# Kernel optimization log

Hardware: AMD Instinct MI355X
Metric: run time of the kernel (lower is better)

The kernel has to match this reference:

```python
import jax, jax.numpy as jnp
import numpy as np

B, T, H, HOR = 512, 256, 256, 22  # batch, seq_len, hidden_size, horizon
IN = 1


def _linear_params(key, fan_in, fan_out):
    kw, kb = jax.random.split(key)
    s = 1.0 / np.sqrt(fan_in)
    w = jax.random.uniform(kw, (fan_in, fan_out), minval=-s, maxval=s, dtype=jnp.float32)
    b = jax.random.uniform(kb, (fan_out,), minval=-s, maxval=s, dtype=jnp.float32)
    return w, b


def setup_inputs() -> dict:
    key = jax.random.key(0)
    ks = jax.random.split(key, 12)
    x = jax.random.normal(ks[0], (B, T, IN), dtype=jnp.float32)
    Wz_w, Wz_b = _linear_params(ks[1], IN, H)
    Uz_w, Uz_b = _linear_params(ks[2], H, H)
    Wr_w, Wr_b = _linear_params(ks[3], IN, H)
    Ur_w, Ur_b = _linear_params(ks[4], H, H)
    Wh_w, Wh_b = _linear_params(ks[5], IN, H)
    Uh_w, Uh_b = _linear_params(ks[6], H, H)
    Wg_w, Wg_b = _linear_params(ks[7], 1, H)
    fc1_w, fc1_b = _linear_params(ks[8], H, H)
    fc2_w, _ = _linear_params(ks[9], H, HOR)
    fc2_w = fc2_w * 0.1                      # model init scales output weight by 0.1
    fc2_b = jnp.full((HOR,), -5.0, dtype=jnp.float32)  # bias.fill_(-5.0)
    return {
        "x": x,
        "Wz_w": Wz_w, "Wz_b": Wz_b, "Uz_w": Uz_w, "Uz_b": Uz_b,
        "Wr_w": Wr_w, "Wr_b": Wr_b, "Ur_w": Ur_w, "Ur_b": Ur_b,
        "Wh_w": Wh_w, "Wh_b": Wh_b, "Uh_w": Uh_w, "Uh_b": Uh_b,
        "Wg_w": Wg_w, "Wg_b": Wg_b,
        "omega_raw": jnp.float32(-8.0), "alpha_raw": jnp.float32(1.0),
        "beta_raw": jnp.float32(1.0), "gamma": jnp.float32(0.4),
        "fc1_w": fc1_w, "fc1_b": fc1_b, "fc2_w": fc2_w, "fc2_b": fc2_b,
    }


def reference(x, Wz_w, Wz_b, Uz_w, Uz_b, Wr_w, Wr_b, Ur_w, Ur_b,
              Wh_w, Wh_b, Uh_w, Uh_b, Wg_w, Wg_b,
              omega_raw, alpha_raw, beta_raw, gamma,
              fc1_w, fc1_b, fc2_w, fc2_b):
    batch = x.shape[0]
    # GARCH reparameterization: omega>0, alpha>=0, beta>=0, alpha+beta<1
    omega = jax.nn.softplus(omega_raw) + 1e-6
    a = jax.nn.sigmoid(alpha_raw)
    b = jax.nn.sigmoid(beta_raw) * (1.0 - a * 0.99)

    # Precompute all input-to-hidden projections (no recurrence dependence)
    xz = jnp.einsum('bti,ih->bth', x, Wz_w) + Wz_b  # (B,T,H)
    xr = jnp.einsum('bti,ih->bth', x, Wr_w) + Wr_b
    xh = jnp.einsum('bti,ih->bth', x, Wh_w) + Wh_b
    eps_seq = x[:, :, 0]                            # (B,T)

    def step(carry, inp):
        h, eps_sq, sig_sq = carry
        xz_t, xr_t, xh_t, eps_t = inp
        garch_in = omega + a * eps_sq + b * sig_sq           # (B,)
        gt = garch_in[:, None] * Wg_w[0] + Wg_b              # Wg: Linear(1,H)
        z = jax.nn.sigmoid(xz_t + h @ Uz_w + Uz_b)
        r = jax.nn.sigmoid(xr_t + h @ Ur_w + Ur_b)
        h_tilde = jnp.tanh(xh_t + (r * h) @ Uh_w + Uh_b)
        h_hat = (1.0 - z) * h_tilde + z * h
        h_new = jnp.tanh(h_hat + gamma * gt)
        return (h_new, eps_t ** 2, garch_in), None

    h0 = jnp.zeros((batch, H), dtype=x.dtype)
    eps0 = jnp.full((batch,), 1e-6, dtype=x.dtype)
    sig0 = jnp.full((batch,), 1e-6, dtype=x.dtype)
    inputs = (jnp.swapaxes(xz, 0, 1), jnp.swapaxes(xr, 0, 1),
              jnp.swapaxes(xh, 0, 1), jnp.swapaxes(eps_seq, 0, 1))
    (h, _, sigma_sq), _ = jax.lax.scan(step, (h0, eps0, sig0), inputs)

    vol_base = jnp.sqrt(sigma_sq + 1e-8)                 # (B,)
    hid = jax.nn.relu(h @ fc1_w + fc1_b)                 # dropout = identity (eval)
    nn_scale = jax.nn.softplus(hid @ fc2_w + fc2_b)      # (B,HOR)
    vol = vol_base[:, None] * (1.0 + nn_scale)
    vol = jnp.clip(vol, 0.01, 10.0)
    return vol, sigma_sq
```

## Files before the change

kernel.cpp:

```cpp
#include <hip/hip_runtime.h>

#define BATCH 512
#define TT 256
#define HH 256
#define HOR 22

__device__ __forceinline__ float bf16lo(unsigned u) { return __uint_as_float(u << 16); }
__device__ __forceinline__ float bf16hi(unsigned u) { return __uint_as_float(u & 0xFFFF0000u); }
__device__ __forceinline__ float rcp_(float x) { return __builtin_amdgcn_rcpf(x); }
__device__ __forceinline__ float sigmoidf_(float x) { return rcp_(1.0f + __expf(-x)); }
__device__ __forceinline__ float tanhf_(float x) {
    float e = __expf(-2.0f * fabsf(x));
    float t = (1.0f - e) * rcp_(1.0f + e);
    return copysignf(t, x);
}
__device__ __forceinline__ unsigned f2bf_rne(float f) {
    unsigned u = __float_as_uint(f);
    unsigned lsb = (u >> 16) & 1u;
    return (u + 0x7FFFu + lsb) >> 16;
}

#define DOT2(acc, a, b) asm("v_dot2_f32_bf16 %0, %1, %2, %0" : "+v"(acc) : "v"(a), "v"(b))

#define PIN(v) asm volatile("" : "+v"(v))
#define PIN4(q) { PIN((q).x); PIN((q).y); PIN((q).z); PIN((q).w); }

#define DPPF(x, ctrl) __int_as_float(__builtin_amdgcn_update_dpp(0, __float_as_int(x), (ctrl), 0xF, 0xF, true))
#define RCOMB(out, a, b, p, ctrl)                          \
    {                                                      \
        float _ta = (a) + DPPF((a), ctrl);                 \
        float _tb = (b) + DPPF((b), ctrl);                 \
        (out) = (p) ? _tb : _ta;                           \
    }
#define RCOMB4(out, a, b, p2v)                                         \
    {                                                                  \
        float _xa = (p2v) ? DPPF((a), 0x114) : DPPF((a), 0x104);       \
        float _xb = (p2v) ? DPPF((b), 0x114) : DPPF((b), 0x104);       \
        float _ta = (a) + _xa;                                         \
        float _tb = (b) + _xb;                                         \
        (out) = (p2v) ? _tb : _ta;                                     \
    }

__global__ __launch_bounds__(256) void prep_kernel(const float* __restrict__ Uz,
                                                   const float* __restrict__ Ur,
                                                   const float* __restrict__ Uh,
                                                   unsigned* __restrict__ UzT,
                                                   unsigned* __restrict__ UrT,
                                                   unsigned* __restrict__ UhT) {
    int tid = blockIdx.x * 256 + threadIdx.x;
    int m  = tid >> 15;
    int r  = tid & 32767;
    int j  = r & 255;
    int kp = r >> 8;
    const float* src = (m == 0) ? Uz : (m == 1) ? Ur : Uh;
    unsigned*    dst = (m == 0) ? UzT : (m == 1) ? UrT : UhT;
    float a0 = src[(2 * kp)     * HH + j];
    float a1 = src[(2 * kp + 1) * HH + j];
    dst[j * (HH / 2) + kp] = f2bf_rne(a0) | (f2bf_rne(a1) << 16);
}

__global__ __launch_bounds__(512) __attribute__((amdgpu_waves_per_eu(2, 2))) void gru_kernel(
    const float* __restrict__ x,
    const float* __restrict__ Wzw, const float* __restrict__ Wzb, const float* __restrict__ Uzb,
    const float* __restrict__ Wrw, const float* __restrict__ Wrb, const float* __restrict__ Urb,
    const float* __restrict__ Whw, const float* __restrict__ Whb, const float* __restrict__ Uhb,
    const float* __restrict__ Wgw, const float* __restrict__ Wgb,
    const float* __restrict__ om_raw, const float* __restrict__ al_raw,
    const float* __restrict__ be_raw, const float* __restrict__ gam,
    const float* __restrict__ fc1w, const float* __restrict__ fc1b,
    const float* __restrict__ fc2w, const float* __restrict__ fc2b,
    const unsigned* __restrict__ UzT, const unsigned* __restrict__ UrT,
    const unsigned* __restrict__ UhT,
    float* __restrict__ out) {
    __shared__ __align__(16) unsigned char hS[2 * 640];
    __shared__ __align__(16) unsigned char rhS[2 * 640];
    __shared__ float xs[2][TT];
    __shared__ float hid[2][HH];

    const int t  = threadIdx.x;
    const int s  = t & 7;
    const int cq = t >> 3;
    const bool p0 = (t & 1), p1 = (t & 2), p2 = (t & 4);
    const int c_own   = t & 3;
    const int b_own   = (t >> 2) & 1;
    const int col_own = 4 * cq + c_own;
    const int b0 = blockIdx.x * 2;

    uint4 wz[4][4], wr[4][4], wh[4][4];
#pragma unroll
    for (int l = 0; l < 4; ++l) {
        const int base = (4 * cq + l) * 128 + s * 16;
        const uint4* pz = (const uint4*)(UzT + base);
        const uint4* pr = (const uint4*)(UrT + base);
        const uint4* ph = (const uint4*)(UhT + base);
#pragma unroll
        for (int u = 0; u < 4; ++u) { wz[l][u] = pz[u]; wr[l][u] = pr[u]; wh[l][u] = ph[u]; }
    }
#pragma unroll
    for (int l = 0; l < 4; ++l) {
#pragma unroll
        for (int u = 0; u < 4; ++u) { PIN4(wz[l][u]); PIN4(wr[l][u]); PIN4(wh[l][u]); }
    }

    const float omega = log1pf(__expf(om_raw[0])) + 1e-6f;
    const float aco   = sigmoidf_(al_raw[0]);
    const float bco   = sigmoidf_(be_raw[0]) * (1.0f - aco * 0.99f);
    const float gma   = gam[0];

    const float wz_o = Wzw[col_own], bz_o = Wzb[col_own] + Uzb[col_own];
    const float wr_o = Wrw[col_own], br_o = Wrb[col_own] + Urb[col_own];
    const float wh_o = Whw[col_own], bh_o = Whb[col_own] + Uhb[col_own];
    const float wg_o = Wgw[col_own], bg_o = Wgb[col_own];

    xs[t >> 8][t & 255] = x[(b0 + (t >> 8)) * TT + (t & 255)];
    if (t < 320) ((unsigned*)hS)[t] = 0;

    float h_own = 0.f, z_own = 0.f;
    float eps0 = 1e-6f, sig0 = 1e-6f, eps1 = 1e-6f, sig1 = 1e-6f;
    __syncthreads();

    const int sl_off = s * 80;
    const int wr_off = (col_own >> 5) * 40 + (col_own & 31);

    for (int tt = 0; tt < TT; ++tt) {
        const float x0 = xs[0][tt];
        const float x1 = xs[1][tt];
        const float g0 = omega + aco * eps0 + bco * sig0;
        const float g1 = omega + aco * eps1 + bco * sig1;
        eps0 = x0 * x0; sig0 = g0;
        eps1 = x1 * x1; sig1 = g1;
        const float x_o = p2 ? x1 : x0;
        const float g_o = p2 ? g1 : g0;

        uint4 ha[4], hb[4];
        {
            const uint4* h0p = (const uint4*)(hS + sl_off);
            const uint4* h1p = (const uint4*)(hS + 640 + sl_off);
#pragma unroll
            for (int u = 0; u < 4; ++u) { ha[u] = h0p[u]; hb[u] = h1p[u]; }
        }
        float az[4][2], ar[4][2];
#pragma unroll
        for (int l = 0; l < 4; ++l) { az[l][0] = 0.f; az[l][1] = 0.f; ar[l][0] = 0.f; ar[l][1] = 0.f; }
#pragma unroll
        for (int l = 0; l < 4; ++l) {
#pragma unroll
            for (int u = 0; u < 4; ++u) {
                uint4 a = wz[l][u], b = wr[l][u];
                DOT2(az[l][0], a.x, ha[u].x); DOT2(az[l][0], a.y, ha[u].y);
                DOT2(az[l][0], a.z, ha[u].z); DOT2(az[l][0], a.w, ha[u].w);
                DOT2(az[l][1], a.x, hb[u].x); DOT2(az[l][1], a.y, hb[u].y);
                DOT2(az[l][1], a.z, hb[u].z); DOT2(az[l][1], a.w, hb[u].w);
                DOT2(ar[l][0], b.x, ha[u].x); DOT2(ar[l][0], b.y, ha[u].y);
                DOT2(ar[l][0], b.z, ha[u].z); DOT2(ar[l][0], b.w, ha[u].w);
                DOT2(ar[l][1], b.x, hb[u].x); DOT2(ar[l][1], b.y, hb[u].y);
                DOT2(ar[l][1], b.z, hb[u].z); DOT2(ar[l][1], b.w, hb[u].w);
            }
        }
        float z1a[2][2], r1a[2][2];
        RCOMB(z1a[0][0], az[0][0], az[1][0], p0, 0xB1);
        RCOMB(z1a[0][1], az[0][1], az[1][1], p0, 0xB1);
        RCOMB(z1a[1][0], az[2][0], az[3][0], p0, 0xB1);
        RCOMB(z1a[1][1], az[2][1], az[3][1], p0, 0xB1);
        RCOMB(r1a[0][0], ar[0][0], ar[1][0], p0, 0xB1);
        RCOMB(r1a[0][1], ar[0][1], ar[1][1], p0, 0xB1);
        RCOMB(r1a[1][0], ar[2][0], ar[3][0], p0, 0xB1);
        RCOMB(r1a[1][1], ar[2][1], ar[3][1], p0, 0xB1);
        float z2a[2], r2a[2];
        RCOMB(z2a[0], z1a[0][0], z1a[1][0], p1, 0x4E);
        RCOMB(z2a[1], z1a[0][1], z1a[1][1], p1, 0x4E);
        RCOMB(r2a[0], r1a[0][0], r1a[1][0], p1, 0x4E);
        RCOMB(r2a[1], r1a[0][1], r1a[1][1], p1, 0x4E);
        float accZ, accR;
        RCOMB4(accZ, z2a[0], z2a[1], p2);
        RCOMB4(accR, r2a[0], r2a[1], p2);

        z_own = sigmoidf_(accZ + x_o * wz_o + bz_o);
        const float r = sigmoidf_(accR + x_o * wr_o + br_o);
        ((unsigned short*)(rhS + b_own * 640))[wr_off] = (unsigned short)f2bf_rne(r * h_own);
        __syncthreads();

        uint4 pa[4], pb[4];
        {
            const uint4* r0p = (const uint4*)(rhS + sl_off);
            const uint4* r1p = (const uint4*)(rhS + 640 + sl_off);
#pragma unroll
            for (int u = 0; u < 4; ++u) { pa[u] = r0p[u]; pb[u] = r1p[u]; }
        }
        float ah[4][2];
#pragma unroll
        for (int l = 0; l < 4; ++l) { ah[l][0] = 0.f; ah[l][1] = 0.f; }
#pragma unroll
        for (int l = 0; l < 4; ++l) {
#pragma unroll
            for (int u = 0; u < 4; ++u) {
                uint4 a = wh[l][u];
                DOT2(ah[l][0], a.x, pa[u].x); DOT2(ah[l][0], a.y, pa[u].y);
                DOT2(ah[l][0], a.z, pa[u].z); DOT2(ah[l][0], a.w, pa[u].w);
                DOT2(ah[l][1], a.x, pb[u].x); DOT2(ah[l][1], a.y, pb[u].y);
                DOT2(ah[l][1], a.z, pb[u].z); DOT2(ah[l][1], a.w, pb[u].w);
            }
        }
        float h1a[2][2];
        RCOMB(h1a[0][0], ah[0][0], ah[1][0], p0, 0xB1);
        RCOMB(h1a[0][1], ah[0][1], ah[1][1], p0, 0xB1);
        RCOMB(h1a[1][0], ah[2][0], ah[3][0], p0, 0xB1);
        RCOMB(h1a[1][1], ah[2][1], ah[3][1], p0, 0xB1);
        float h2a[2];
        RCOMB(h2a[0], h1a[0][0], h1a[1][0], p1, 0x4E);
        RCOMB(h2a[1], h1a[0][1], h1a[1][1], p1, 0x4E);
        float accH;
        RCOMB4(accH, h2a[0], h2a[1], p2);

        const float htld = tanhf_(accH + x_o * wh_o + bh_o);
        const float hh   = (1.f - z_own) * htld + z_own * h_own;
        const float hn   = tanhf_(hh + gma * (g_o * wg_o + bg_o));
        h_own = hn;
        ((unsigned short*)(hS + b_own * 640))[wr_off] = (unsigned short)f2bf_rne(hn);
        __syncthreads();
    }

    xs[b_own][col_own] = h_own;
    __syncthreads();

    {
        const int b = t >> 8, j = t & 255;
        float acc = 0.f;
#pragma unroll 4
        for (int k = 0; k < HH; ++k) acc += xs[b][k] * fc1w[k * HH + j];
        hid[b][j] = fmaxf(acc + fc1b[j], 0.f);
    }
    __syncthreads();

    if (t < 2 * HOR) {
        const int b = t / HOR;
        const int c = t % HOR;
        float acc = fc2b[c];
        for (int k = 0; k < HH; ++k) acc += hid[b][k] * fc2w[k * HOR + c];
        const float sp = log1pf(__expf(acc));
        const float sg = b ? sig1 : sig0;
        const float vb = sqrtf(sg + 1e-8f);
        float vol = vb * (1.0f + sp);
        vol = fminf(fmaxf(vol, 0.01f), 10.0f);
        out[(b0 + b) * HOR + c] = vol;
    }
    if (t == 0) out[BATCH * HOR + b0]     = sig0;
    if (t == 1) out[BATCH * HOR + b0 + 1] = sig1;
}

extern "C" void kernel_launch(void* const* d_in, const int* in_sizes, int n_in,
                              void* d_out, int out_size, void* d_ws, size_t ws_size,
                              hipStream_t stream) {
    const float* x    = (const float*)d_in[0];
    const float* Wzw  = (const float*)d_in[1];
    const float* Wzb  = (const float*)d_in[2];
    const float* Uzw  = (const float*)d_in[3];
    const float* Uzb  = (const float*)d_in[4];
    const float* Wrw  = (const float*)d_in[5];
    const float* Wrb  = (const float*)d_in[6];
    const float* Urw  = (const float*)d_in[7];
    const float* Urb  = (const float*)d_in[8];
    const float* Whw  = (const float*)d_in[9];
    const float* Whb  = (const float*)d_in[10];
    const float* Uhw  = (const float*)d_in[11];
    const float* Uhb  = (const float*)d_in[12];
    const float* Wgw  = (const float*)d_in[13];
    const float* Wgb  = (const float*)d_in[14];
    const float* om   = (const float*)d_in[15];
    const float* al   = (const float*)d_in[16];
    const float* be   = (const float*)d_in[17];
    const float* ga   = (const float*)d_in[18];
    const float* fc1w = (const float*)d_in[19];
    const float* fc1b = (const float*)d_in[20];
    const float* fc2w = (const float*)d_in[21];
    const float* fc2b = (const float*)d_in[22];

    unsigned* UzT = (unsigned*)d_ws;
    unsigned* UrT = UzT + 32768;
    unsigned* UhT = UrT + 32768;

    prep_kernel<<<384, 256, 0, stream>>>(Uzw, Urw, Uhw, UzT, UrT, UhT);
    gru_kernel<<<256, 512, 0, stream>>>(x, Wzw, Wzb, Uzb, Wrw, Wrb, Urb, Whw, Whb, Uhb,
                                        Wgw, Wgb, om, al, be, ga, fc1w, fc1b, fc2w, fc2b,
                                        UzT, UrT, UhT, (float*)d_out);
}
```

Before: 780.3 us.

## Double threads per block, keep Uz/Ur in registers and stream Uh from cache

After: 1.216 ms. 55.8% more time.

```diff
diff --git a/kernel.cpp b/kernel.cpp
--- a/kernel.cpp
+++ b/kernel.cpp
@@ -5,8 +5,6 @@
 #define HH 256
 #define HOR 22
 
-__device__ __forceinline__ float bf16lo(unsigned u) { return __uint_as_float(u << 16); }
-__device__ __forceinline__ float bf16hi(unsigned u) { return __uint_as_float(u & 0xFFFF0000u); }
 __device__ __forceinline__ float rcp_(float x) { return __builtin_amdgcn_rcpf(x); }
 __device__ __forceinline__ float sigmoidf_(float x) { return rcp_(1.0f + __expf(-x)); }
 __device__ __forceinline__ float tanhf_(float x) {
@@ -21,6 +19,13 @@
 }
 
 #define DOT2(acc, a, b) asm("v_dot2_f32_bf16 %0, %1, %2, %0" : "+v"(acc) : "v"(a), "v"(b))
+#define DOT2Q(accv, wq, hq)               \
+    {                                     \
+        DOT2(accv, (wq).x, (hq).x);       \
+        DOT2(accv, (wq).y, (hq).y);       \
+        DOT2(accv, (wq).z, (hq).z);       \
+        DOT2(accv, (wq).w, (hq).w);       \
+    }
 
 #define PIN(v) asm volatile("" : "+v"(v))
 #define PIN4(q) { PIN((q).x); PIN((q).y); PIN((q).z); PIN((q).w); }
@@ -32,13 +37,10 @@
         float _tb = (b) + DPPF((b), ctrl);                 \
         (out) = (p) ? _tb : _ta;                           \
     }
-#define RCOMB4(out, a, b, p2v)                                         \
+#define SUM4(out, a, p2v)                                              \
     {                                                                  \
-        float _xa = (p2v) ? DPPF((a), 0x114) : DPPF((a), 0x104);       \
-        float _xb = (p2v) ? DPPF((b), 0x114) : DPPF((b), 0x104);       \
-        float _ta = (a) + _xa;                                         \
-        float _tb = (b) + _xb;                                         \
-        (out) = (p2v) ? _tb : _ta;                                     \
+        float _x = (p2v) ? DPPF((a), 0x114) : DPPF((a), 0x104);        \
+        (out) = (a) + _x;                                              \
     }
 
 __global__ __launch_bounds__(256) void prep_kernel(const float* __restrict__ Uz,
@@ -59,7 +61,7 @@
     dst[j * (HH / 2) + kp] = f2bf_rne(a0) | (f2bf_rne(a1) << 16);
 }
 
-__global__ __launch_bounds__(512) __attribute__((amdgpu_waves_per_eu(2, 2))) void gru_kernel(
+__global__ __launch_bounds__(1024) void gru_kernel(
     const float* __restrict__ x,
     const float* __restrict__ Wzw, const float* __restrict__ Wzb, const float* __restrict__ Uzb,
     const float* __restrict__ Wrw, const float* __restrict__ Wrb, const float* __restrict__ Urb,
@@ -77,30 +79,29 @@
     __shared__ float xs[2][TT];
     __shared__ float hid[2][HH];
 
-    const int t  = threadIdx.x;
-    const int s  = t & 7;
-    const int cq = t >> 3;
-    const bool p0 = (t & 1), p1 = (t & 2), p2 = (t & 4);
-    const int c_own   = t & 3;
-    const int b_own   = (t >> 2) & 1;
-    const int col_own = 4 * cq + c_own;
+    const int t    = threadIdx.x;
+    const int s    = t & 7;
+    const int cp   = t >> 3;
+    const int col0 = 2 * cp;
+    const bool p0 = (s & 1), p1 = (s & 2), p2 = (s & 4);
+    const int b_own   = s & 1;
+    const int col_own = col0 + ((s >> 1) & 1);
     const int b0 = blockIdx.x * 2;
 
-    uint4 wz[4][4], wr[4][4], wh[4][4];
-#pragma unroll
-    for (int l = 0; l < 4; ++l) {
-        const int base = (4 * cq + l) * 128 + s * 16;
-        const uint4* pz = (const uint4*)(UzT + base);
-        const uint4* pr = (const uint4*)(UrT + base);
-        const uint4* ph = (const uint4*)(UhT + base);
-#pragma unroll
-        for (int u = 0; u < 4; ++u) { wz[l][u] = pz[u]; wr[l][u] = pr[u]; wh[l][u] = ph[u]; }
-    }
-#pragma unroll
-    for (int l = 0; l < 4; ++l) {
-#pragma unroll
-        for (int u = 0; u < 4; ++u) { PIN4(wz[l][u]); PIN4(wr[l][u]); PIN4(wh[l][u]); }
-    }
+    uint4 wz[2][4], wr[2][4];
+    {
+        const uint4* pz = (const uint4*)(UzT + col0 * 128 + s * 16);
+        const uint4* pr = (const uint4*)(UrT + col0 * 128 + s * 16);
+#pragma unroll
+        for (int u = 0; u < 4; ++u) {
+            wz[0][u] = pz[u];      wz[1][u] = pz[32 + u];
+            wr[0][u] = pr[u];      wr[1][u] = pr[32 + u];
+        }
+    }
+#pragma unroll
+    for (int c = 0; c < 2; ++c)
+#pragma unroll
+        for (int u = 0; u < 4; ++u) { PIN4(wz[c][u]); PIN4(wr[c][u]); }
 
     const float omega = log1pf(__expf(om_raw[0])) + 1e-6f;
     const float aco   = sigmoidf_(al_raw[0]);
@@ -112,15 +113,16 @@
     const float wh_o = Whw[col_own], bh_o = Whb[col_own] + Uhb[col_own];
     const float wg_o = Wgw[col_own], bg_o = Wgb[col_own];
 
-    xs[t >> 8][t & 255] = x[(b0 + (t >> 8)) * TT + (t & 255)];
+    if (t < 512) xs[t >> 8][t & 255] = x[(b0 + (t >> 8)) * TT + (t & 255)];
     if (t < 320) ((unsigned*)hS)[t] = 0;
 
-    float h_own = 0.f, z_own = 0.f;
+    float h_own = 0.f;
     float eps0 = 1e-6f, sig0 = 1e-6f, eps1 = 1e-6f, sig1 = 1e-6f;
     __syncthreads();
 
-    const int sl_off = s * 80;
-    const int wr_off = (col_own >> 5) * 40 + (col_own & 31);
+    const unsigned* uhb   = UhT + col0 * 128 + s * 16;
+    const int       sl    = s * 80;
+    const int       wroff = (col_own >> 5) * 40 + (col_own & 31);
 
     for (int tt = 0; tt < TT; ++tt) {
         const float x0 = xs[0][tt];
@@ -129,101 +131,109 @@
         const float g1 = omega + aco * eps1 + bco * sig1;
         eps0 = x0 * x0; sig0 = g0;
         eps1 = x1 * x1; sig1 = g1;
-        const float x_o = p2 ? x1 : x0;
-        const float g_o = p2 ? g1 : g0;
-
-        uint4 ha[4], hb[4];
-        {
-            const uint4* h0p = (const uint4*)(hS + sl_off);
-            const uint4* h1p = (const uint4*)(hS + 640 + sl_off);
-#pragma unroll
-            for (int u = 0; u < 4; ++u) { ha[u] = h0p[u]; hb[u] = h1p[u]; }
-        }
-        float az[4][2], ar[4][2];
-#pragma unroll
-        for (int l = 0; l < 4; ++l) { az[l][0] = 0.f; az[l][1] = 0.f; ar[l][0] = 0.f; ar[l][1] = 0.f; }
-#pragma unroll
-        for (int l = 0; l < 4; ++l) {
-#pragma unroll
-            for (int u = 0; u < 4; ++u) {
-                uint4 a = wz[l][u], b = wr[l][u];
-                DOT2(az[l][0], a.x, ha[u].x); DOT2(az[l][0], a.y, ha[u].y);
-                DOT2(az[l][0], a.z, ha[u].z); DOT2(az[l][0], a.w, ha[u].w);
-                DOT2(az[l][1], a.x, hb[u].x); DOT2(az[l][1], a.y, hb[u].y);
-                DOT2(az[l][1], a.z, hb[u].z); DOT2(az[l][1], a.w, hb[u].w);
-                DOT2(ar[l][0], b.x, ha[u].x); DOT2(ar[l][0], b.y, ha[u].y);
-                DOT2(ar[l][0], b.z, ha[u].z); DOT2(ar[l][0], b.w, ha[u].w);
-                DOT2(ar[l][1], b.x, hb[u].x); DOT2(ar[l][1], b.y, hb[u].y);
-                DOT2(ar[l][1], b.z, hb[u].z); DOT2(ar[l][1], b.w, hb[u].w);
-            }
-        }
-        float z1a[2][2], r1a[2][2];
-        RCOMB(z1a[0][0], az[0][0], az[1][0], p0, 0xB1);
-        RCOMB(z1a[0][1], az[0][1], az[1][1], p0, 0xB1);
-        RCOMB(z1a[1][0], az[2][0], az[3][0], p0, 0xB1);
-        RCOMB(z1a[1][1], az[2][1], az[3][1], p0, 0xB1);
-        RCOMB(r1a[0][0], ar[0][0], ar[1][0], p0, 0xB1);
-        RCOMB(r1a[0][1], ar[0][1], ar[1][1], p0, 0xB1);
-        RCOMB(r1a[1][0], ar[2][0], ar[3][0], p0, 0xB1);
-        RCOMB(r1a[1][1], ar[2][1], ar[3][1], p0, 0xB1);
-        float z2a[2], r2a[2];
-        RCOMB(z2a[0], z1a[0][0], z1a[1][0], p1, 0x4E);
-        RCOMB(z2a[1], z1a[0][1], z1a[1][1], p1, 0x4E);
-        RCOMB(r2a[0], r1a[0][0], r1a[1][0], p1, 0x4E);
-        RCOMB(r2a[1], r1a[0][1], r1a[1][1], p1, 0x4E);
+        const float x_o = p0 ? x1 : x0;
+        const float g_o = p0 ? g1 : g0;
+
+        unsigned lz = 0;
+        asm volatile("" : "+v"(lz));
+        const uint4* q0p = (const uint4*)(uhb + lz);
+        const uint4* q1p = (const uint4*)(uhb + 128 + lz);
+        uint4 u0[4], u1[4];
+#pragma unroll
+        for (int u = 0; u < 4; ++u) u0[u] = q0p[u];
+
+        float az[2][2], ar[2][2];
+        az[0][0]=az[0][1]=az[1][0]=az[1][1]=0.f;
+        ar[0][0]=ar[0][1]=ar[1][0]=ar[1][1]=0.f;
+        {
+            const uint4* hp = (const uint4*)(hS + sl);
+            uint4 hq[4];
+#pragma unroll
+            for (int u = 0; u < 4; ++u) hq[u] = hp[u];
+#pragma unroll
+            for (int u = 0; u < 4; ++u) {
+                DOT2Q(az[0][0], wz[0][u], hq[u]);
+                DOT2Q(az[1][0], wz[1][u], hq[u]);
+                DOT2Q(ar[0][0], wr[0][u], hq[u]);
+                DOT2Q(ar[1][0], wr[1][u], hq[u]);
+            }
+        }
+#pragma unroll
+        for (int u = 0; u < 4; ++u) u1[u] = q1p[u];
+        {
+            const uint4* hp = (const uint4*)(hS + 640 + sl);
+            uint4 hq[4];
+#pragma unroll
+            for (int u = 0; u < 4; ++u) hq[u] = hp[u];
+#pragma unroll
+            for (int u = 0; u < 4; ++u) {
+                DOT2Q(az[0][1], wz[0][u], hq[u]);
+                DOT2Q(az[1][1], wz[1][u], hq[u]);
+                DOT2Q(ar[0][1], wr[0][u], hq[u]);
+                DOT2Q(ar[1][1], wr[1][u], hq[u]);
+            }
+        }
+
+        float zc0, zc1, rc0, rc1;
+        RCOMB(zc0, az[0][0], az[0][1], p0, 0xB1);
+        RCOMB(zc1, az[1][0], az[1][1], p0, 0xB1);
+        RCOMB(rc0, ar[0][0], ar[0][1], p0, 0xB1);
+        RCOMB(rc1, ar[1][0], ar[1][1], p0, 0xB1);
+        float z2, r2;
+        RCOMB(z2, zc0, zc1, p1, 0x4E);
+        RCOMB(r2, rc0, rc1, p1, 0x4E);
         float accZ, accR;
-        RCOMB4(accZ, z2a[0], z2a[1], p2);
-        RCOMB4(accR, r2a[0], r2a[1], p2);
-
-        z_own = sigmoidf_(accZ + x_o * wz_o + bz_o);
-        const float r = sigmoidf_(accR + x_o * wr_o + br_o);
-        ((unsigned short*)(rhS + b_own * 640))[wr_off] = (unsigned short)f2bf_rne(r * h_own);
+        SUM4(accZ, z2, p2);
+        SUM4(accR, r2, p2);
+
+        const float z_own = sigmoidf_(accZ + x_o * wz_o + bz_o);
+        const float r     = sigmoidf_(accR + x_o * wr_o + br_o);
+        ((unsigned short*)(rhS + b_own * 640))[wroff] = (unsigned short)f2bf_rne(r * h_own);
         __syncthreads();
 
-        uint4 pa[4], pb[4];
-        {
-            const uint4* r0p = (const uint4*)(rhS + sl_off);
-            const uint4* r1p = (const uint4*)(rhS + 640 + sl_off);
-#pragma unroll
-            for (int u = 0; u < 4; ++u) { pa[u] = r0p[u]; pb[u] = r1p[u]; }
-        }
-        float ah[4][2];
-#pragma unroll
-        for (int l = 0; l < 4; ++l) { ah[l][0] = 0.f; ah[l][1] = 0.f; }
-#pragma unroll
-        for (int l = 0; l < 4; ++l) {
-#pragma unroll
-            for (int u = 0; u < 4; ++u) {
-                uint4 a = wh[l][u];
-                DOT2(ah[l][0], a.x, pa[u].x); DOT2(ah[l][0], a.y, pa[u].y);
-                DOT2(ah[l][0], a.z, pa[u].z); DOT2(ah[l][0], a.w, pa[u].w);
-                DOT2(ah[l][1], a.x, pb[u].x); DOT2(ah[l][1], a.y, pb[u].y);
-                DOT2(ah[l][1], a.z, pb[u].z); DOT2(ah[l][1], a.w, pb[u].w);
-            }
-        }
-        float h1a[2][2];
-        RCOMB(h1a[0][0], ah[0][0], ah[1][0], p0, 0xB1);
-        RCOMB(h1a[0][1], ah[0][1], ah[1][1], p0, 0xB1);
-        RCOMB(h1a[1][0], ah[2][0], ah[3][0], p0, 0xB1);
-        RCOMB(h1a[1][1], ah[2][1], ah[3][1], p0, 0xB1);
-        float h2a[2];
-        RCOMB(h2a[0], h1a[0][0], h1a[1][0], p1, 0x4E);
-        RCOMB(h2a[1], h1a[0][1], h1a[1][1], p1, 0x4E);
+        float ah[2][2];
+        ah[0][0]=ah[0][1]=ah[1][0]=ah[1][1]=0.f;
+        {
+            const uint4* pp = (const uint4*)(rhS + sl);
+            uint4 q[4];
+#pragma unroll
+            for (int u = 0; u < 4; ++u) q[u] = pp[u];
+#pragma unroll
+            for (int u = 0; u < 4; ++u) {
+                DOT2Q(ah[0][0], u0[u], q[u]);
+                DOT2Q(ah[1][0], u1[u], q[u]);
+            }
+        }
+        {
+            const uint4* pp = (const uint4*)(rhS + 640 + sl);
+            uint4 q[4];
+#pragma unroll
+            for (int u = 0; u < 4; ++u) q[u] = pp[u];
+#pragma unroll
+            for (int u = 0; u < 4; ++u) {
+                DOT2Q(ah[0][1], u0[u], q[u]);
+                DOT2Q(ah[1][1], u1[u], q[u]);
+            }
+        }
+        float hc0, hc1, h2;
+        RCOMB(hc0, ah[0][0], ah[0][1], p0, 0xB1);
+        RCOMB(hc1, ah[1][0], ah[1][1], p0, 0xB1);
+        RCOMB(h2, hc0, hc1, p1, 0x4E);
         float accH;
-        RCOMB4(accH, h2a[0], h2a[1], p2);
+        SUM4(accH, h2, p2);
 
         const float htld = tanhf_(accH + x_o * wh_o + bh_o);
         const float hh   = (1.f - z_own) * htld + z_own * h_own;
         const float hn   = tanhf_(hh + gma * (g_o * wg_o + bg_o));
         h_own = hn;
-        ((unsigned short*)(hS + b_own * 640))[wr_off] = (unsigned short)f2bf_rne(hn);
+        ((unsigned short*)(hS + b_own * 640))[wroff] = (unsigned short)f2bf_rne(hn);
         __syncthreads();
     }
 
     xs[b_own][col_own] = h_own;
     __syncthreads();
 
-    {
+    if (t < 512) {
         const int b = t >> 8, j = t & 255;
         float acc = 0.f;
 #pragma unroll 4
@@ -280,7 +290,7 @@
     unsigned* UhT = UrT + 32768;
 
     prep_kernel<<<384, 256, 0, stream>>>(Uzw, Urw, Uhw, UzT, UrT, UhT);
-    gru_kernel<<<256, 512, 0, stream>>>(x, Wzw, Wzb, Uzb, Wrw, Wrb, Urb, Whw, Whb, Uhb,
-                                        Wgw, Wgb, om, al, be, ga, fc1w, fc1b, fc2w, fc2b,
-                                        UzT, UrT, UhT, (float*)d_out);
-}
+    gru_kernel<<<256, 1024, 0, stream>>>(x, Wzw, Wzb, Uzb, Wrw, Wrb, Urb, Whw, Whb, Uhb,
+                                         Wgw, Wgb, om, al, be, ga, fc1w, fc1b, fc2w, fc2b,
+                                         UzT, UrT, UhT, (float*)d_out);
+}
```

## Move Ur weights to AGPRs and Uh weights to LDS to cut VGPR pressure

Applied to the files above, without the earlier changes.

Measured after the change: 909.0 us. 16.5% more time.

```diff
diff --git a/kernel.cpp b/kernel.cpp
--- a/kernel.cpp
+++ b/kernel.cpp
@@ -5,8 +5,6 @@
 #define HH 256
 #define HOR 22
 
-__device__ __forceinline__ float bf16lo(unsigned u) { return __uint_as_float(u << 16); }
-__device__ __forceinline__ float bf16hi(unsigned u) { return __uint_as_float(u & 0xFFFF0000u); }
 __device__ __forceinline__ float rcp_(float x) { return __builtin_amdgcn_rcpf(x); }
 __device__ __forceinline__ float sigmoidf_(float x) { return rcp_(1.0f + __expf(-x)); }
 __device__ __forceinline__ float tanhf_(float x) {
@@ -24,6 +22,9 @@
 
 #define PIN(v) asm volatile("" : "+v"(v))
 #define PIN4(q) { PIN((q).x); PIN((q).y); PIN((q).z); PIN((q).w); }
+
+#define AWRITE(ag, v) asm volatile("v_accvgpr_write_b32 %0, %1" : "=a"(ag) : "v"(v))
+#define AREAD(v, ag)  asm volatile("v_accvgpr_read_b32 %0, %1" : "=v"(v) : "a"(ag))
 
 #define DPPF(x, ctrl) __int_as_float(__builtin_amdgcn_update_dpp(0, __float_as_int(x), (ctrl), 0xF, 0xF, true))
 #define RCOMB(out, a, b, p, ctrl)                          \
@@ -72,6 +73,7 @@
     const unsigned* __restrict__ UzT, const unsigned* __restrict__ UrT,
     const unsigned* __restrict__ UhT,
     float* __restrict__ out) {
+    __shared__ unsigned Uh_lds[32768];
     __shared__ __align__(16) unsigned char hS[2 * 640];
     __shared__ __align__(16) unsigned char rhS[2 * 640];
     __shared__ float xs[2][TT];
@@ -86,20 +88,36 @@
     const int col_own = 4 * cq + c_own;
     const int b0 = blockIdx.x * 2;
 
-    uint4 wz[4][4], wr[4][4], wh[4][4];
+    uint4 wz[4][4];
 #pragma unroll
     for (int l = 0; l < 4; ++l) {
-        const int base = (4 * cq + l) * 128 + s * 16;
-        const uint4* pz = (const uint4*)(UzT + base);
-        const uint4* pr = (const uint4*)(UrT + base);
-        const uint4* ph = (const uint4*)(UhT + base);
-#pragma unroll
-        for (int u = 0; u < 4; ++u) { wz[l][u] = pz[u]; wr[l][u] = pr[u]; wh[l][u] = ph[u]; }
-    }
+        const uint4* pz = (const uint4*)(UzT + (4 * cq + l) * 128 + s * 16);
+#pragma unroll
+        for (int u = 0; u < 4; ++u) wz[l][u] = pz[u];
+    }
+#pragma unroll
+    for (int l = 0; l < 4; ++l)
+#pragma unroll
+        for (int u = 0; u < 4; ++u) PIN4(wz[l][u]);
+
+    unsigned ra[4][4][4];
 #pragma unroll
     for (int l = 0; l < 4; ++l) {
-#pragma unroll
-        for (int u = 0; u < 4; ++u) { PIN4(wz[l][u]); PIN4(wr[l][u]); PIN4(wh[l][u]); }
+        const uint4* pr = (const uint4*)(UrT + (4 * cq + l) * 128 + s * 16);
+#pragma unroll
+        for (int u = 0; u < 4; ++u) {
+            uint4 v = pr[u];
+            AWRITE(ra[l][u][0], v.x);
+            AWRITE(ra[l][u][1], v.y);
+            AWRITE(ra[l][u][2], v.z);
+            AWRITE(ra[l][u][3], v.w);
+        }
+    }
+
+#pragma unroll 4
+    for (int i = 0; i < 64; ++i) {
+        int g = t + 512 * i;
+        Uh_lds[(g & 127) * 256 + (g >> 7)] = UhT[g];
     }
 
     const float omega = log1pf(__expf(om_raw[0])) + 1e-6f;
@@ -121,6 +139,10 @@
 
     const int sl_off = s * 80;
     const int wr_off = (col_own >> 5) * 40 + (col_own & 31);
+
+    const uint4* uhp = ((const uint4*)Uh_lds) + s * 1024 + cq;
+    const uint4* rq0 = (const uint4*)(((const unsigned*)rhS) + s * 20);
+    const uint4* rq1 = (const uint4*)(((const unsigned*)(rhS + 640)) + s * 20);
 
     for (int tt = 0; tt < TT; ++tt) {
         const float x0 = xs[0][tt];
@@ -132,29 +154,34 @@
         const float x_o = p2 ? x1 : x0;
         const float g_o = p2 ? g1 : g0;
 
-        uint4 ha[4], hb[4];
+        const uint4* h0p = (const uint4*)(hS + sl_off);
+        const uint4* h1p = (const uint4*)(hS + 640 + sl_off);
+        float az[4][2], ar[4][2];
+#pragma unroll
+        for (int l = 0; l < 4; ++l) { az[l][0] = 0.f; az[l][1] = 0.f; ar[l][0] = 0.f; ar[l][1] = 0.f; }
         {
-            const uint4* h0p = (const uint4*)(hS + sl_off);
-            const uint4* h1p = (const uint4*)(hS + 640 + sl_off);
-#pragma unroll
-            for (int u = 0; u < 4; ++u) { ha[u] = h0p[u]; hb[u] = h1p[u]; }
-        }
-        float az[4][2], ar[4][2];
-#pragma unroll
-        for (int l = 0; l < 4; ++l) { az[l][0] = 0.f; az[l][1] = 0.f; ar[l][0] = 0.f; ar[l][1] = 0.f; }
-#pragma unroll
-        for (int l = 0; l < 4; ++l) {
+            uint4 hqa = h0p[0], hqb = h1p[0];
 #pragma unroll
             for (int u = 0; u < 4; ++u) {
-                uint4 a = wz[l][u], b = wr[l][u];
-                DOT2(az[l][0], a.x, ha[u].x); DOT2(az[l][0], a.y, ha[u].y);
-                DOT2(az[l][0], a.z, ha[u].z); DOT2(az[l][0], a.w, ha[u].w);
-                DOT2(az[l][1], a.x, hb[u].x); DOT2(az[l][1], a.y, hb[u].y);
-                DOT2(az[l][1], a.z, hb[u].z); DOT2(az[l][1], a.w, hb[u].w);
-                DOT2(ar[l][0], b.x, ha[u].x); DOT2(ar[l][0], b.y, ha[u].y);
-                DOT2(ar[l][0], b.z, ha[u].z); DOT2(ar[l][0], b.w, ha[u].w);
-                DOT2(ar[l][1], b.x, hb[u].x); DOT2(ar[l][1], b.y, hb[u].y);
-                DOT2(ar[l][1], b.z, hb[u].z); DOT2(ar[l][1], b.w, hb[u].w);
+                uint4 ca = hqa, cb = hqb;
+                if (u < 3) { hqa = h0p[u + 1]; hqb = h1p[u + 1]; }
+#pragma unroll
+                for (int l = 0; l < 4; ++l) {
+                    uint4 a = wz[l][u];
+                    DOT2(az[l][0], a.x, ca.x); DOT2(az[l][0], a.y, ca.y);
+                    DOT2(az[l][0], a.z, ca.z); DOT2(az[l][0], a.w, ca.w);
+                    DOT2(az[l][1], a.x, cb.x); DOT2(az[l][1], a.y, cb.y);
+                    DOT2(az[l][1], a.z, cb.z); DOT2(az[l][1], a.w, cb.w);
+                    unsigned t0, t1, t2, t3;
+                    AREAD(t0, ra[l][u][0]);
+                    DOT2(ar[l][0], t0, ca.x); DOT2(ar[l][1], t0, cb.x);
+                    AREAD(t1, ra[l][u][1]);
+                    DOT2(ar[l][0], t1, ca.y); DOT2(ar[l][1], t1, cb.y);
+                    AREAD(t2, ra[l][u][2]);
+                    DOT2(ar[l][0], t2, ca.z); DOT2(ar[l][1], t2, cb.z);
+                    AREAD(t3, ra[l][u][3]);
+                    DOT2(ar[l][0], t3, ca.w); DOT2(ar[l][1], t3, cb.w);
+                }
             }
         }
         float z1a[2][2], r1a[2][2];
@@ -180,25 +207,22 @@
         ((unsigned short*)(rhS + b_own * 640))[wr_off] = (unsigned short)f2bf_rne(r * h_own);
         __syncthreads();
 
-        uint4 pa[4], pb[4];
-        {
-            const uint4* r0p = (const uint4*)(rhS + sl_off);
-            const uint4* r1p = (const uint4*)(rhS + 640 + sl_off);
-#pragma unroll
-            for (int u = 0; u < 4; ++u) { pa[u] = r0p[u]; pb[u] = r1p[u]; }
-        }
         float ah[4][2];
 #pragma unroll
         for (int l = 0; l < 4; ++l) { ah[l][0] = 0.f; ah[l][1] = 0.f; }
 #pragma unroll
-        for (int l = 0; l < 4; ++l) {
-#pragma unroll
-            for (int u = 0; u < 4; ++u) {
-                uint4 a = wh[l][u];
-                DOT2(ah[l][0], a.x, pa[u].x); DOT2(ah[l][0], a.y, pa[u].y);
-                DOT2(ah[l][0], a.z, pa[u].z); DOT2(ah[l][0], a.w, pa[u].w);
-                DOT2(ah[l][1], a.x, pb[u].x); DOT2(ah[l][1], a.y, pb[u].y);
-                DOT2(ah[l][1], a.z, pb[u].z); DOT2(ah[l][1], a.w, pb[u].w);
+        for (int half = 0; half < 2; ++half) {
+            uint4 qa0 = rq0[2 * half], qb0 = rq0[2 * half + 1];
+            uint4 qa1 = rq1[2 * half], qb1 = rq1[2 * half + 1];
+            unsigned r0v[8] = {qa0.x, qa0.y, qa0.z, qa0.w, qb0.x, qb0.y, qb0.z, qb0.w};
+            unsigned r1v[8] = {qa1.x, qa1.y, qa1.z, qa1.w, qb1.x, qb1.y, qb1.z, qb1.w};
+#pragma unroll
+            for (int i = 0; i < 8; ++i) {
+                uint4 w4 = uhp[(8 * half + i) * 64];
+                DOT2(ah[0][0], w4.x, r0v[i]); DOT2(ah[1][0], w4.y, r0v[i]);
+                DOT2(ah[2][0], w4.z, r0v[i]); DOT2(ah[3][0], w4.w, r0v[i]);
+                DOT2(ah[0][1], w4.x, r1v[i]); DOT2(ah[1][1], w4.y, r1v[i]);
+                DOT2(ah[2][1], w4.z, r1v[i]); DOT2(ah[3][1], w4.w, r1v[i]);
             }
         }
         float h1a[2][2];
```
